# Performance work log

Measured on AMD Instinct MI355X. Metric: run time of the kernel, lower is better.

Reference implementation:

```python
import jax, jax.numpy as jnp
import numpy as np

B, T, D, H = 8, 1024, 1024, 16
DH = D // H
EPS = 1e-5


def setup_inputs() -> dict:
    key = jax.random.key(0)
    ks = jax.random.split(key, 8)
    s = 0.02
    return {
        "x": jax.random.normal(ks[0], (B, T, D), dtype=jnp.float32),
        # per-head Q/K/V weights stacked: (H, in_c, d_head), applied as x @ W
        "Wq": jax.random.normal(ks[1], (H, D, DH), dtype=jnp.float32) * s,
        "Wk": jax.random.normal(ks[2], (H, D, DH), dtype=jnp.float32) * s,
        "Wv": jax.random.normal(ks[3], (H, D, DH), dtype=jnp.float32) * s,
        # FFN weights stored (in, out): y = x @ W
        "W1": jax.random.normal(ks[4], (D, D), dtype=jnp.float32) * s,
        "W2": jax.random.normal(ks[5], (D, D), dtype=jnp.float32) * s,
        "g1": jnp.ones((D,), jnp.float32),
        "b1": jnp.zeros((D,), jnp.float32),
        "g2": jnp.ones((D,), jnp.float32),
        "b2": jnp.zeros((D,), jnp.float32),
    }


def _layer_norm(x, g, b):
    m = jnp.mean(x, axis=-1, keepdims=True)
    v = jnp.mean((x - m) ** 2, axis=-1, keepdims=True)  # biased, as torch LN
    return (x - m) * jax.lax.rsqrt(v + EPS) * g + b


def reference(x, Wq, Wk, Wv, W1, W2, g1, b1, g2, b2):
    b, t, d = x.shape
    dh = Wq.shape[-1]
    q = jnp.einsum("btc,hcd->bhtd", x, Wq)
    k = jnp.einsum("btc,hcd->bhtd", x, Wk)
    v = jnp.einsum("btc,hcd->bhtd", x, Wv)
    attn = jnp.einsum("bhtd,bhsd->bhts", q, k) / (dh ** 0.5)
    # Original: attn @ ones(T,T) -> every column equals rowsum(attn);
    # softmax(dim=1) over the query axis is then constant across columns,
    # so out[t] = softmax_t(rowsum)[t] * sum_s v[s]. Same math, reduced.
    rowsum = attn.sum(axis=-1)               # (B,H,T)
    p = jax.nn.softmax(rowsum, axis=-1)      # softmax over query index t
    vsum = v.sum(axis=2)                     # (B,H,DH)
    head_out = p[..., None] * vsum[:, :, None, :]        # (B,H,T,DH)
    out = head_out.transpose(0, 2, 1, 3).reshape(b, t, d)  # concat heads
    x1 = _layer_norm(x + out, g1, b1)
    ff = jax.nn.relu(x1 @ W1) @ W2           # dropout = identity (eval)
    return _layer_norm(x1 + ff, g2, b2)
```

## Files before the change

### kernel.cpp

```cpp
#include <hip/hip_runtime.h>

#define NB 8
#define NT 1024
#define ND 1024
#define NH 16
#define NDH 64
#define NM (NB*NT)
#define LNEPS 1e-5f

typedef __attribute__((ext_vector_type(8))) __bf16 bf16x8;
typedef __attribute__((ext_vector_type(4))) float f32x4;

__global__ void transpose_to_bf16(const float* __restrict__ W1, const float* __restrict__ W2,
                                  __bf16* __restrict__ WT1, __bf16* __restrict__ WT2) {
    __shared__ float tile[32][33];
    const float* W = blockIdx.z ? W2 : W1;
    __bf16* WT = blockIdx.z ? WT2 : WT1;
    int bx = blockIdx.x * 32;
    int by = blockIdx.y * 32;
    int tx = threadIdx.x;
    int ty = threadIdx.y;
    for (int i = ty; i < 32; i += 8)
        tile[i][tx] = W[(size_t)(by + i) * ND + bx + tx];
    __syncthreads();
    for (int i = ty; i < 32; i += 8)
        WT[(size_t)(bx + i) * ND + by + tx] = (__bf16)tile[tx][i];
}

__global__ void xsum_kernel(const float* __restrict__ x, float* __restrict__ xsum) {
    int b = blockIdx.x;
    int chunk = blockIdx.y;
    int tid = threadIdx.x;
    const float4* xp = (const float4*)(x + ((size_t)b * NT + chunk * 16) * ND) + tid;
    float4 s = {0.f, 0.f, 0.f, 0.f};
    #pragma unroll
    for (int t = 0; t < 16; ++t) {
        float4 v = xp[(size_t)t * (ND / 4)];
        s.x += v.x; s.y += v.y; s.z += v.z; s.w += v.w;
    }
    float* dst = xsum + b * ND + tid * 4;
    atomicAdd(dst + 0, s.x);
    atomicAdd(dst + 1, s.y);
    atomicAdd(dst + 2, s.z);
    atomicAdd(dst + 3, s.w);
}

__global__ void head_prep(const float* __restrict__ xsum,
                          const float* __restrict__ Wq, const float* __restrict__ Wk,
                          const float* __restrict__ Wv,
                          float* __restrict__ vsum, float* __restrict__ wqk) {
    int h = blockIdx.x, b = blockIdx.y;
    int t = threadIdx.x;
    int d = t & 63, q = t >> 6;
    __shared__ float part[2][4][NDH];
    __shared__ float ks[NDH];
    const float* xs = xsum + b * ND;
    float sk = 0.f, sv = 0.f;
    for (int c = q * 256; c < q * 256 + 256; ++c) {
        float xv = xs[c];
        sk += xv * Wk[((size_t)h * ND + c) * NDH + d];
        sv += xv * Wv[((size_t)h * ND + c) * NDH + d];
    }
    part[0][q][d] = sk;
    part[1][q][d] = sv;
    __syncthreads();
    if (t < 64) {
        ks[t] = part[0][0][t] + part[0][1][t] + part[0][2][t] + part[0][3][t];
    } else if (t < 128) {
        int dd = t - 64;
        vsum[((size_t)b * NH + h) * NDH + dd] =
            part[1][0][dd] + part[1][1][dd] + part[1][2][dd] + part[1][3][dd];
    }
    __syncthreads();
    for (int c = t; c < ND; c += 256) {
        const float* wq = Wq + ((size_t)h * ND + c) * NDH;
        float s = 0.f;
        #pragma unroll 16
        for (int dd = 0; dd < NDH; ++dd) s += wq[dd] * ks[dd];
        wqk[((size_t)b * NH + h) * ND + c] = s * 0.125f;
    }
}

__global__ __launch_bounds__(256) void rowsum_kernel(const float* __restrict__ x,
                                                     const float* __restrict__ wqk,
                                                     float* __restrict__ rowsum) {
    int tc = blockIdx.x, b = blockIdx.y;
    int tid = threadIdx.x, wid = tid >> 6, lane = tid & 63;
    int t0 = tc * 16 + wid * 4;
    float acc[4][16];
    #pragma unroll
    for (int tq = 0; tq < 4; ++tq)
        #pragma unroll
        for (int h = 0; h < 16; ++h) acc[tq][h] = 0.f;
    const float4* wb = (const float4*)(wqk + (size_t)b * NH * ND);
    #pragma unroll
    for (int chunk = 0; chunk < 4; ++chunk) {
        float4 xv[4];
        #pragma unroll
        for (int tq = 0; tq < 4; ++tq)
            xv[tq] = ((const float4*)(x + ((size_t)b * NT + t0 + tq) * ND))[chunk * 64 + lane];
        #pragma unroll
        for (int h = 0; h < 16; ++h) {
            float4 wv = wb[h * 256 + chunk * 64 + lane];
            #pragma unroll
            for (int tq = 0; tq < 4; ++tq)
                acc[tq][h] += xv[tq].x * wv.x + xv[tq].y * wv.y +
                              xv[tq].z * wv.z + xv[tq].w * wv.w;
        }
    }
    bool c0 = lane & 1, c1 = lane & 2, c2 = lane & 4, c3 = lane & 8;
    float out4[4];
    #pragma unroll
    for (int tq = 0; tq < 4; ++tq) {
        float w8[8];
        #pragma unroll
        for (int j = 0; j < 8; ++j) {
            float send = c0 ? acc[tq][2 * j] : acc[tq][2 * j + 1];
            float recv = __shfl_xor(send, 1, 64);
            w8[j] = (c0 ? acc[tq][2 * j + 1] : acc[tq][2 * j]) + recv;
        }
        float u4[4];
        #pragma unroll
        for (int j = 0; j < 4; ++j) {
            float send = c1 ? w8[2 * j] : w8[2 * j + 1];
            float recv = __shfl_xor(send, 2, 64);
            u4[j] = (c1 ? w8[2 * j + 1] : w8[2 * j]) + recv;
        }
        float s2[2];
        #pragma unroll
        for (int j = 0; j < 2; ++j) {
            float send = c2 ? u4[2 * j] : u4[2 * j + 1];
            float recv = __shfl_xor(send, 4, 64);
            s2[j] = (c2 ? u4[2 * j + 1] : u4[2 * j]) + recv;
        }
        float send = c3 ? s2[0] : s2[1];
        float recv = __shfl_xor(send, 8, 64);
        float r = (c3 ? s2[1] : s2[0]) + recv;
        r += __shfl_xor(r, 16, 64);
        r += __shfl_xor(r, 32, 64);
        out4[tq] = r;
    }
    if (lane < 16) {
        float4 o = {out4[0], out4[1], out4[2], out4[3]};
        *(float4*)(rowsum + ((size_t)b * NH + lane) * NT + t0) = o;
    }
}

__global__ void softmax_kernel(float* __restrict__ rs) {
    int bh = blockIdx.x, tid = threadIdx.x;
    int wave = tid >> 6, lane = tid & 63;
    float* row = rs + (size_t)bh * NT;
    float4 v = ((float4*)row)[tid];
    float m = fmaxf(fmaxf(v.x, v.y), fmaxf(v.z, v.w));
    __shared__ float red[4];
    for (int off = 32; off; off >>= 1) m = fmaxf(m, __shfl_down(m, off, 64));
    if (lane == 0) red[wave] = m;
    __syncthreads();
    m = fmaxf(fmaxf(red[0], red[1]), fmaxf(red[2], red[3]));
    __syncthreads();
    float4 e;
    e.x = __expf(v.x - m); e.y = __expf(v.y - m);
    e.z = __expf(v.z - m); e.w = __expf(v.w - m);
    float s = e.x + e.y + e.z + e.w;
    for (int off = 32; off; off >>= 1) s += __shfl_down(s, off, 64);
    if (lane == 0) red[wave] = s;
    __syncthreads();
    s = red[0] + red[1] + red[2] + red[3];
    float inv = 1.f / s;
    e.x *= inv; e.y *= inv; e.z *= inv; e.w *= inv;
    ((float4*)row)[tid] = e;
}

__global__ void ln1_kernel(const float* __restrict__ x, const float* __restrict__ p,
                           const float* __restrict__ vsum,
                           const float* __restrict__ g1, const float* __restrict__ b1,
                           __bf16* __restrict__ x1b) {
    int t = blockIdx.x, b = blockIdx.y, tid = threadIdx.x;
    int wave = tid >> 6, lane = tid & 63;
    size_t rowoff = ((size_t)b * NT + t) * ND;
    float4 xv = ((const float4*)(x + rowoff))[tid];
    int h = tid >> 4;
    float pv = p[((size_t)b * NH + h) * NT + t];
    float4 vs = ((const float4*)(vsum + ((size_t)b * NH + h) * NDH))[tid & 15];
    float4 s;
    s.x = xv.x + pv * vs.x; s.y = xv.y + pv * vs.y;
    s.z = xv.z + pv * vs.z; s.w = xv.w + pv * vs.w;
    float sum = s.x + s.y + s.z + s.w;
    float sq = s.x * s.x + s.y * s.y + s.z * s.z + s.w * s.w;
    __shared__ float rs_[4], rq_[4];
    for (int off = 32; off; off >>= 1) {
        sum += __shfl_down(sum, off, 64);
        sq += __shfl_down(sq, off, 64);
    }
    if (lane == 0) { rs_[wave] = sum; rq_[wave] = sq; }
    __syncthreads();
    sum = rs_[0] + rs_[1] + rs_[2] + rs_[3];
    sq = rq_[0] + rq_[1] + rq_[2] + rq_[3];
    float mu = sum * (1.f / ND);
    float var = sq * (1.f / ND) - mu * mu;
    float rstd = rsqrtf(var + LNEPS);
    float4 g = ((const float4*)g1)[tid];
    float4 bb = ((const float4*)b1)[tid];
    union { __bf16 h4[4]; uint2 u; } pk;
    pk.h4[0] = (__bf16)((s.x - mu) * rstd * g.x + bb.x);
    pk.h4[1] = (__bf16)((s.y - mu) * rstd * g.y + bb.y);
    pk.h4[2] = (__bf16)((s.z - mu) * rstd * g.z + bb.z);
    pk.h4[3] = (__bf16)((s.w - mu) * rstd * g.w + bb.w);
    ((uint2*)(x1b + rowoff))[tid] = pk.u;
}

template <int RELU>
__global__ __launch_bounds__(256) void gemm_bf16(const __bf16* __restrict__ A,
                                                 const __bf16* __restrict__ BT,
                                                 __bf16* __restrict__ Cout) {
    const int K = 1024, N = 1024;
    __shared__ __bf16 As[128][32];
    __shared__ __bf16 Bs[128][32];
    int raw = blockIdx.x;
    int swz = (raw & 7) * 64 + (raw >> 3);
    int m0 = (swz >> 3) * 128;
    int n0 = (swz & 7) * 128;
    int tid = threadIdx.x;
    int wid = tid >> 6, lane = tid & 63;
    int wr = wid >> 1, wc = wid & 1;
    int r = lane & 15, g = lane >> 4;
    int srow = wid * 32 + (lane >> 2);
    int skoff = (lane & 3) * 8;
    const __bf16* Ag = A + (size_t)(m0 + srow) * K + skoff;
    const __bf16* Bg = BT + (size_t)(n0 + srow) * K + skoff;
    f32x4 acc[4][4] = {};
    for (int k0 = 0; k0 < K; k0 += 32) {
        __syncthreads();
        __builtin_amdgcn_global_load_lds(
            (const __attribute__((address_space(1))) unsigned int*)(Ag + k0),
            (__attribute__((address_space(3))) unsigned int*)&As[wid * 32][0], 16, 0, 0);
        __builtin_amdgcn_global_load_lds(
            (const __attribute__((address_space(1))) unsigned int*)(Ag + (size_t)16 * K + k0),
            (__attribute__((address_space(3))) unsigned int*)&As[wid * 32 + 16][0], 16, 0, 0);
        __builtin_amdgcn_global_load_lds(
            (const __attribute__((address_space(1))) unsigned int*)(Bg + k0),
            (__attribute__((address_space(3))) unsigned int*)&Bs[wid * 32][0], 16, 0, 0);
        __builtin_amdgcn_global_load_lds(
            (const __attribute__((address_space(1))) unsigned int*)(Bg + (size_t)16 * K + k0),
            (__attribute__((address_space(3))) unsigned int*)&Bs[wid * 32 + 16][0], 16, 0, 0);
        __syncthreads();
        bf16x8 af[4], bf[4];
        #pragma unroll
        for (int mf = 0; mf < 4; ++mf)
            af[mf] = *(const bf16x8*)&As[wr * 64 + mf * 16 + r][g * 8];
        #pragma unroll
        for (int nf = 0; nf < 4; ++nf)
            bf[nf] = *(const bf16x8*)&Bs[wc * 64 + nf * 16 + r][g * 8];
        #pragma unroll
        for (int mf = 0; mf < 4; ++mf)
            #pragma unroll
            for (int nf = 0; nf < 4; ++nf)
                acc[mf][nf] = __builtin_amdgcn_mfma_f32_16x16x32_bf16(af[mf], bf[nf], acc[mf][nf], 0, 0, 0);
    }
    #pragma unroll
    for (int mf = 0; mf < 4; ++mf) {
        #pragma unroll
        for (int nf = 0; nf < 4; ++nf) {
            int col = n0 + wc * 64 + nf * 16 + r;
            #pragma unroll
            for (int i = 0; i < 4; ++i) {
                int row = m0 + wr * 64 + mf * 16 + g * 4 + i;
                float v = acc[mf][nf][i];
                if (RELU) v = fmaxf(v, 0.f);
                Cout[(size_t)row * N + col] = (__bf16)v;
            }
        }
    }
}

__global__ void ln2_kernel(const __bf16* __restrict__ x1b, const __bf16* __restrict__ ffb,
                           float* __restrict__ out,
                           const float* __restrict__ g2, const float* __restrict__ b2) {
    int t = blockIdx.x, b = blockIdx.y, tid = threadIdx.x;
    int wave = tid >> 6, lane = tid & 63;
    size_t rowoff = ((size_t)b * NT + t) * ND;
    union { __bf16 h4[4]; uint2 u; } pk, pf;
    pk.u = ((const uint2*)(x1b + rowoff))[tid];
    pf.u = ((const uint2*)(ffb + rowoff))[tid];
    float4 s;
    s.x = (float)pk.h4[0] + (float)pf.h4[0];
    s.y = (float)pk.h4[1] + (float)pf.h4[1];
    s.z = (float)pk.h4[2] + (float)pf.h4[2];
    s.w = (float)pk.h4[3] + (float)pf.h4[3];
    float sum = s.x + s.y + s.z + s.w;
    float sq = s.x * s.x + s.y * s.y + s.z * s.z + s.w * s.w;
    __shared__ float rs_[4], rq_[4];
    for (int off = 32; off; off >>= 1) {
        sum += __shfl_down(sum, off, 64);
        sq += __shfl_down(sq, off, 64);
    }
    if (lane == 0) { rs_[wave] = sum; rq_[wave] = sq; }
    __syncthreads();
    sum = rs_[0] + rs_[1] + rs_[2] + rs_[3];
    sq = rq_[0] + rq_[1] + rq_[2] + rq_[3];
    float mu = sum * (1.f / ND);
    float var = sq * (1.f / ND) - mu * mu;
    float rstd = rsqrtf(var + LNEPS);
    float4 g = ((const float4*)g2)[tid];
    float4 bb = ((const float4*)b2)[tid];
    float4 o;
    o.x = (s.x - mu) * rstd * g.x + bb.x;
    o.y = (s.y - mu) * rstd * g.y + bb.y;
    o.z = (s.z - mu) * rstd * g.z + bb.z;
    o.w = (s.w - mu) * rstd * g.w + bb.w;
    ((float4*)(out + rowoff))[tid] = o;
}

extern "C" void kernel_launch(void* const* d_in, const int* in_sizes, int n_in,
                              void* d_out, int out_size, void* d_ws, size_t ws_size,
                              hipStream_t stream) {
    const float* x  = (const float*)d_in[0];
    const float* Wq = (const float*)d_in[1];
    const float* Wk = (const float*)d_in[2];
    const float* Wv = (const float*)d_in[3];
    const float* W1 = (const float*)d_in[4];
    const float* W2 = (const float*)d_in[5];
    const float* g1 = (const float*)d_in[6];
    const float* b1 = (const float*)d_in[7];
    const float* g2 = (const float*)d_in[8];
    const float* b2 = (const float*)d_in[9];
    float* out = (float*)d_out;

    char* w = (char*)d_ws;
    float* xsum = (float*)w;   w += (size_t)NB * ND * 4;
    float* vsum = (float*)w;   w += (size_t)NB * NH * NDH * 4;
    float* wqk  = (float*)w;   w += (size_t)NB * NH * ND * 4;
    float* rsum = (float*)w;   w += (size_t)NB * NH * NT * 4;
    __bf16* x1b = (__bf16*)w;  w += (size_t)NM * ND * 2;
    __bf16* h1b = (__bf16*)w;  w += (size_t)NM * ND * 2;
    __bf16* ffb = (__bf16*)w;  w += (size_t)NM * ND * 2;
    __bf16* w1t = (__bf16*)w;  w += (size_t)ND * ND * 2;
    __bf16* w2t = (__bf16*)w;  w += (size_t)ND * ND * 2;

    hipMemsetAsync(xsum, 0, (size_t)NB * ND * 4, stream);

    transpose_to_bf16<<<dim3(32, 32, 2), dim3(32, 8), 0, stream>>>(W1, W2, w1t, w2t);

    xsum_kernel<<<dim3(NB, 64), 256, 0, stream>>>(x, xsum);
    head_prep<<<dim3(NH, NB), 256, 0, stream>>>(xsum, Wq, Wk, Wv, vsum, wqk);
    rowsum_kernel<<<dim3(64, NB), 256, 0, stream>>>(x, wqk, rsum);
    softmax_kernel<<<NB * NH, 256, 0, stream>>>(rsum);
    ln1_kernel<<<dim3(NT, NB), 256, 0, stream>>>(x, rsum, vsum, g1, b1, x1b);

    gemm_bf16<1><<<512, 256, 0, stream>>>(x1b, w1t, h1b);
    gemm_bf16<0><<<512, 256, 0, stream>>>(h1b, w2t, ffb);
    ln2_kernel<<<dim3(NT, NB), 256, 0, stream>>>(x1b, ffb, out, g2, b2);
}
```

Baseline: 232.8 us.

## Double GEMM K-tile to 64 with XOR-swizzled LDS layout

```diff
diff --git a/kernel.cpp b/kernel.cpp
--- a/kernel.cpp
+++ b/kernel.cpp
@@ -56,6 +56,7 @@
     __shared__ float ks[NDH];
     const float* xs = xsum + b * ND;
     float sk = 0.f, sv = 0.f;
+    #pragma unroll 4
     for (int c = q * 256; c < q * 256 + 256; ++c) {
         float xv = xs[c];
         sk += xv * Wk[((size_t)h * ND + c) * NDH + d];
@@ -214,8 +215,8 @@
                                                  const __bf16* __restrict__ BT,
                                                  __bf16* __restrict__ Cout) {
     const int K = 1024, N = 1024;
-    __shared__ __bf16 As[128][32];
-    __shared__ __bf16 Bs[128][32];
+    __shared__ __bf16 As[128 * 64];
+    __shared__ __bf16 Bs[128 * 64];
     int raw = blockIdx.x;
     int swz = (raw & 7) * 64 + (raw >> 3);
     int m0 = (swz >> 3) * 128;
@@ -224,38 +225,40 @@
     int wid = tid >> 6, lane = tid & 63;
     int wr = wid >> 1, wc = wid & 1;
     int r = lane & 15, g = lane >> 4;
-    int srow = wid * 32 + (lane >> 2);
-    int skoff = (lane & 3) * 8;
-    const __bf16* Ag = A + (size_t)(m0 + srow) * K + skoff;
-    const __bf16* Bg = BT + (size_t)(n0 + srow) * K + skoff;
+    int srow = tid >> 3;
+    int soff_e = (((tid & 7) * 16) ^ ((srow & 7) << 4)) >> 1;
+    const __bf16* Ag = A + (size_t)(m0 + srow) * K + soff_e;
+    const __bf16* Bg = BT + (size_t)(n0 + srow) * K + soff_e;
+    int swz_r = (r & 7) << 4;
     f32x4 acc[4][4] = {};
-    for (int k0 = 0; k0 < K; k0 += 32) {
+    for (int k0 = 0; k0 < K; k0 += 64) {
         __syncthreads();
-        __builtin_amdgcn_global_load_lds(
-            (const __attribute__((address_space(1))) unsigned int*)(Ag + k0),
-            (__attribute__((address_space(3))) unsigned int*)&As[wid * 32][0], 16, 0, 0);
-        __builtin_amdgcn_global_load_lds(
-            (const __attribute__((address_space(1))) unsigned int*)(Ag + (size_t)16 * K + k0),
-            (__attribute__((address_space(3))) unsigned int*)&As[wid * 32 + 16][0], 16, 0, 0);
-        __builtin_amdgcn_global_load_lds(
-            (const __attribute__((address_space(1))) unsigned int*)(Bg + k0),
-            (__attribute__((address_space(3))) unsigned int*)&Bs[wid * 32][0], 16, 0, 0);
-        __builtin_amdgcn_global_load_lds(
-            (const __attribute__((address_space(1))) unsigned int*)(Bg + (size_t)16 * K + k0),
-            (__attribute__((address_space(3))) unsigned int*)&Bs[wid * 32 + 16][0], 16, 0, 0);
+        #pragma unroll
+        for (int j = 0; j < 4; ++j) {
+            __builtin_amdgcn_global_load_lds(
+                (const __attribute__((address_space(1))) unsigned int*)(Ag + (size_t)(j * 32) * K + k0),
+                (__attribute__((address_space(3))) unsigned int*)&As[(j * 32 + wid * 8) * 64], 16, 0, 0);
+            __builtin_amdgcn_global_load_lds(
+                (const __attribute__((address_space(1))) unsigned int*)(Bg + (size_t)(j * 32) * K + k0),
+                (__attribute__((address_space(3))) unsigned int*)&Bs[(j * 32 + wid * 8) * 64], 16, 0, 0);
+        }
         __syncthreads();
-        bf16x8 af[4], bf[4];
-        #pragma unroll
-        for (int mf = 0; mf < 4; ++mf)
-            af[mf] = *(const bf16x8*)&As[wr * 64 + mf * 16 + r][g * 8];
-        #pragma unroll
-        for (int nf = 0; nf < 4; ++nf)
-            bf[nf] = *(const bf16x8*)&Bs[wc * 64 + nf * 16 + r][g * 8];
-        #pragma unroll
-        for (int mf = 0; mf < 4; ++mf)
+        #pragma unroll
+        for (int ks = 0; ks < 2; ++ks) {
+            int ob = (ks * 64 + g * 16) ^ swz_r;
+            bf16x8 af[4], bf[4];
+            #pragma unroll
+            for (int mf = 0; mf < 4; ++mf)
+                af[mf] = *(const bf16x8*)((const char*)&As[(wr * 64 + mf * 16 + r) * 64] + ob);
             #pragma unroll
             for (int nf = 0; nf < 4; ++nf)
-                acc[mf][nf] = __builtin_amdgcn_mfma_f32_16x16x32_bf16(af[mf], bf[nf], acc[mf][nf], 0, 0, 0);
+                bf[nf] = *(const bf16x8*)((const char*)&Bs[(wc * 64 + nf * 16 + r) * 64] + ob);
+            #pragma unroll
+            for (int mf = 0; mf < 4; ++mf)
+                #pragma unroll
+                for (int nf = 0; nf < 4; ++nf)
+                    acc[mf][nf] = __builtin_amdgcn_mfma_f32_16x16x32_bf16(af[mf], bf[nf], acc[mf][nf], 0, 0, 0);
+        }
     }
     #pragma unroll
     for (int mf = 0; mf < 4; ++mf) {
```

New measurement: 240.6 us. 3.4% more time.
